# Kernel optimization log

Measured on AMD Instinct MI355X. Metric: run time of the kernel, lower is better.

Reference implementation:

```python
import jax, jax.numpy as jnp
import numpy as np

B, H, W = 16, 1024, 1024
EPS = 1e-7
FG_PROB = 0.1  # foreground pixel probability for synthetic gt


def setup_inputs() -> dict:
    key = jax.random.key(0)
    k1, k2 = jax.random.split(key)
    probs = jax.random.normal(k1, (B, 2, H, W), dtype=jnp.float32)
    gt = (jax.random.uniform(k2, (B, H, W)) < FG_PROB).astype(jnp.float32)
    gt_f_num = gt.sum(axis=(1, 2))  # per-sample foreground pixel count (float)
    return {"probs": probs, "gt": gt, "gt_f_num": gt_f_num, "img_h": H, "img_w": W}


def reference(probs, gt, gt_f_num, img_h, img_w):
    # foreground probability, clamped
    pc = jax.nn.softmax(probs, axis=1)[:, 1, :, :]
    pc = jnp.clip(pc, EPS, 1.0 - EPS)
    b = pc.shape[0]
    f_loss = -(gt * jnp.log(pc)).reshape(b, -1)          # [B, N]
    b_loss = -((1.0 - gt) * jnp.log(1.0 - pc)).reshape(b, -1)  # [B, N]
    n = b_loss.shape[1]

    # sort background loss descending per sample; top gt_f_num[i] entries are
    # "difficult" negatives, the rest are "simple" (equivalent to the torch
    # gather-into-zero-buffers since only sums/counts are taken afterwards)
    sorted_b = -jnp.sort(-b_loss, axis=1)                # descending, [B, N]
    k = gt_f_num.astype(jnp.int32)                       # int(gt_f_num[i])
    mask = jnp.arange(n, dtype=jnp.int32)[None, :] < k[:, None]  # [B, N]

    difficult_sum = jnp.sum(jnp.where(mask, sorted_b, 0.0), axis=1)
    simple_sum = jnp.sum(jnp.where(mask, 0.0, sorted_b), axis=1)
    difficult_num = jnp.sum(mask & (sorted_b != 0.0), axis=1).astype(jnp.float32)

    difficult_b_loss = difficult_sum / (difficult_num + 1e-16)
    simple_b_loss = simple_sum / (float(img_h * img_w) + 1e-16)
    f_loss_mean = f_loss.sum(axis=1) / (gt_f_num + 1e-16)

    return difficult_b_loss.mean() + f_loss_mean.mean() + simple_b_loss.mean()
```

## Files before the change

kernel.cpp:

```cpp
#include <hip/hip_runtime.h>
#include <math.h>

#define NB 16
#define NPIX 1048576
#define BINS 2048
#define CHUNKS 128
#define TPB_A 512
#define PIX_PER_BLOCK (NPIX / CHUNKS)
#define PPT 16
#define ITERS (PIX_PER_BLOCK / (TPB_A * 4))
#define REPL 8
#define TPB_B 256
#define BINS_PER_CHUNK (BINS / TPB_B)
#define D_LO   (-10.24f)
#define D_SCALE (100.0f)
#define D_BIAS  (1024.0f)
#define BINW_D  (0.01f)

__global__ __launch_bounds__(TPB_A) void pass_a(
    const float* __restrict__ probs, const float* __restrict__ gt,
    unsigned* __restrict__ g_cnt)
{
    __shared__ unsigned s_cnt[BINS];

    const int tid = threadIdx.x;
    #pragma unroll
    for (int j = 0; j < BINS / TPB_A; ++j) s_cnt[j * TPB_A + tid] = 0u;
    __syncthreads();

    const int blk = blockIdx.x;
    const int b = blk / CHUNKS;
    const int chunk = blk % CHUNKS;
    const float* p0 = probs + (size_t)b * 2 * NPIX;
    const float* p1 = p0 + NPIX;
    const float* gp = gt + (size_t)b * NPIX;
    const int base = chunk * PIX_PER_BLOCK;

    #pragma unroll
    for (int it = 0; it < ITERS; ++it) {
        const int i = base + ((it * TPB_A + tid) << 2);
        const float4 v0 = *(const float4*)(p0 + i);
        const float4 v1 = *(const float4*)(p1 + i);
        const float4 vg = *(const float4*)(gp + i);
        const float dv[4] = {v1.x - v0.x, v1.y - v0.y, v1.z - v0.z, v1.w - v0.w};
        const float gv[4] = {vg.x, vg.y, vg.z, vg.w};
        #pragma unroll
        for (int c = 0; c < 4; ++c) {
            int bin = (int)fmaf(dv[c], D_SCALE, D_BIAS);
            bin = bin < 0 ? 0 : (bin > BINS - 1 ? BINS - 1 : bin);
            const unsigned inc = (gv[c] > 0.5f) ? 0x10000u : 1u;
            atomicAdd(&s_cnt[bin], inc);
        }
    }
    __syncthreads();

    unsigned* dst = g_cnt + ((size_t)b * REPL + (chunk & (REPL - 1))) * BINS;
    #pragma unroll
    for (int j = 0; j < BINS / TPB_A; ++j) {
        const int bin = j * TPB_A + tid;
        const unsigned c = s_cnt[bin];
        if (c) atomicAdd(&dst[bin], c);
    }
}

__device__ __forceinline__ float softplus_ref(float m) {
    return fmaxf(m, 0.f) + log1pf(__expf(-fabsf(m)));
}

__global__ __launch_bounds__(TPB_B) void pass_b(
    const unsigned* __restrict__ g_cnt, const float* __restrict__ gt_f_num,
    float* __restrict__ terms)
{
    __shared__ unsigned s_cnt[BINS];
    __shared__ unsigned s_suf[TPB_B];
    __shared__ double s_wsuf[TPB_B];
    __shared__ double s_fred[TPB_B];
    __shared__ double s_dsum;

    const int b = blockIdx.x;
    const int t = threadIdx.x;

    #pragma unroll
    for (int j = 0; j < BINS_PER_CHUNK; ++j) {
        const int bin = j * TPB_B + t;
        unsigned c = 0;
        #pragma unroll
        for (int r = 0; r < REPL; ++r)
            c += g_cnt[((size_t)b * REPL + r) * BINS + bin];
        s_cnt[bin] = c;
    }
    __syncthreads();

    unsigned c = 0; double w = 0.0, f = 0.0;
    const int cb = t * BINS_PER_CHUNK;
    #pragma unroll
    for (int j = 0; j < BINS_PER_CHUNK; ++j) {
        const unsigned pk = s_cnt[cb + j];
        const unsigned bg = pk & 0xFFFFu, fg = pk >> 16;
        const float m = fmaf((float)(cb + j) + 0.5f, BINW_D, D_LO);
        const float sp = softplus_ref(m);
        c += bg;
        w += (double)bg * (double)sp;
        f += (double)fg * (double)(sp - m);
    }
    s_suf[t] = c; s_wsuf[t] = w; s_fred[t] = f;
    __syncthreads();

    for (int off = 1; off < TPB_B; off <<= 1) {
        const unsigned ac = (t + off < TPB_B) ? s_suf[t + off] : 0u;
        const double aw = (t + off < TPB_B) ? s_wsuf[t + off] : 0.0;
        const double af = (t + off < TPB_B) ? s_fred[t + off] : 0.0;
        __syncthreads();
        s_suf[t] += ac; s_wsuf[t] += aw; s_fred[t] += af;
        __syncthreads();
    }

    const long long kk = (long long)gt_f_num[b];
    const unsigned long long n_pos = (unsigned long long)s_suf[0];
    const unsigned long long suf_me = s_suf[t];
    const unsigned long long suf_nx = (t + 1 < TPB_B) ? s_suf[t + 1] : 0ull;

    if (kk > 0 && (unsigned long long)kk < n_pos &&
        suf_nx < (unsigned long long)kk && (unsigned long long)kk <= suf_me) {
        unsigned long long cum = suf_nx;
        double W = (t + 1 < TPB_B) ? s_wsuf[t + 1] : 0.0;
        int bstar = cb;
        for (int j = BINS_PER_CHUNK - 1; j >= 0; --j) {
            const int bin = cb + j;
            const unsigned bg = s_cnt[bin] & 0xFFFFu;
            if (cum + bg >= (unsigned long long)kk) { bstar = bin; break; }
            cum += bg;
            const float m = fmaf((float)bin + 0.5f, BINW_D, D_LO);
            W += (double)bg * (double)softplus_ref(m);
        }
        const double partial = (double)(kk - (long long)cum);
        const float mstar = fmaf((float)bstar + 0.5f, BINW_D, D_LO);
        s_dsum = W + partial * (double)softplus_ref(mstar);
    }
    __syncthreads();

    if (t == 0) {
        const double S_total = s_wsuf[0];
        const double fs = s_fred[0];
        const double gfn = (double)gt_f_num[b];
        double dsum, dnum;
        if (kk <= 0) { dsum = 0.0; dnum = 0.0; }
        else if ((unsigned long long)kk >= n_pos) { dsum = S_total; dnum = (double)n_pos; }
        else { dsum = s_dsum; dnum = (double)kk; }
        const double term = dsum / (dnum + 1e-16)
                          + fs / (gfn + 1e-16)
                          + (S_total - dsum) / ((double)NPIX + 1e-16);
        terms[b] = (float)term;
    }
}

__global__ void pass_c(const float* __restrict__ terms, float* __restrict__ out)
{
    if (threadIdx.x == 0 && blockIdx.x == 0) {
        float s = 0.f;
        #pragma unroll
        for (int i = 0; i < NB; ++i) s += terms[i];
        out[0] = s / (float)NB;
    }
}

extern "C" void kernel_launch(void* const* d_in, const int* in_sizes, int n_in,
                              void* d_out, int out_size, void* d_ws, size_t ws_size,
                              hipStream_t stream) {
    const float* probs = (const float*)d_in[0];
    const float* gt    = (const float*)d_in[1];
    const float* gfn   = (const float*)d_in[2];
    char* ws = (char*)d_ws;

    const size_t hist_bytes = (size_t)NB * REPL * BINS * 4;
    unsigned* g_cnt = (unsigned*)ws;
    float*    terms = (float*)(ws + hist_bytes);

    hipMemsetAsync(ws, 0, hist_bytes, stream);

    hipLaunchKernelGGL(pass_a, dim3(NB * CHUNKS), dim3(TPB_A), 0, stream,
                       probs, gt, g_cnt);
    hipLaunchKernelGGL(pass_b, dim3(NB), dim3(TPB_B), 0, stream,
                       g_cnt, gfn, terms);
    hipLaunchKernelGGL(pass_c, dim3(1), dim3(64), 0, stream,
                       terms, (float*)d_out);
}
```

Baseline: 248.5 us.

## Compute loss sums exactly per pixel and histogram only a narrow background band

```diff
diff --git a/kernel.cpp b/kernel.cpp
--- a/kernel.cpp
+++ b/kernel.cpp
@@ -3,29 +3,35 @@
 
 #define NB 16
 #define NPIX 1048576
-#define BINS 2048
 #define CHUNKS 128
 #define TPB_A 512
 #define PIX_PER_BLOCK (NPIX / CHUNKS)
-#define PPT 16
 #define ITERS (PIX_PER_BLOCK / (TPB_A * 4))
 #define REPL 8
 #define TPB_B 256
-#define BINS_PER_CHUNK (BINS / TPB_B)
-#define D_LO   (-10.24f)
-#define D_SCALE (100.0f)
-#define D_BIAS  (1024.0f)
-#define BINW_D  (0.01f)
+#define BBINS 2048
+#define BINS_PER_CHUNK (BBINS / TPB_B)
+#define BAND_LO 0.9f
+#define BAND_HI 3.1f
+#define BSCALE ((float)BBINS / (BAND_HI - BAND_LO))
+#define BINW_B ((BAND_HI - BAND_LO) / (float)BBINS)
+#define B_CAP 16.636f
+#define F_CAP 16.1181f
+
+__device__ __forceinline__ void fadd_glb(float* p, float v) {
+    __hip_atomic_fetch_add(p, v, __ATOMIC_RELAXED, __HIP_MEMORY_SCOPE_AGENT);
+}
 
 __global__ __launch_bounds__(TPB_A) void pass_a(
     const float* __restrict__ probs, const float* __restrict__ gt,
-    unsigned* __restrict__ g_cnt)
+    unsigned* __restrict__ g_hist, float* __restrict__ g_scal)
 {
-    __shared__ unsigned s_cnt[BINS];
+    __shared__ unsigned s_hist[BBINS];
+    __shared__ float s_red[4][TPB_A / 64];
 
     const int tid = threadIdx.x;
     #pragma unroll
-    for (int j = 0; j < BINS / TPB_A; ++j) s_cnt[j * TPB_A + tid] = 0u;
+    for (int j = 0; j < BBINS / TPB_A; ++j) s_hist[j * TPB_A + tid] = 0u;
     __syncthreads();
 
     const int blk = blockIdx.x;
@@ -36,6 +42,8 @@
     const float* gp = gt + (size_t)b * NPIX;
     const int base = chunk * PIX_PER_BLOCK;
 
+    float f_acc = 0.f, b_acc = 0.f, shi_acc = 0.f, chi_acc = 0.f;
+
     #pragma unroll
     for (int it = 0; it < ITERS; ++it) {
         const int i = base + ((it * TPB_A + tid) << 2);
@@ -46,35 +54,60 @@
         const float gv[4] = {vg.x, vg.y, vg.z, vg.w};
         #pragma unroll
         for (int c = 0; c < 4; ++c) {
-            int bin = (int)fmaf(dv[c], D_SCALE, D_BIAS);
-            bin = bin < 0 ? 0 : (bin > BINS - 1 ? BINS - 1 : bin);
-            const unsigned inc = (gv[c] > 0.5f) ? 0x10000u : 1u;
-            atomicAdd(&s_cnt[bin], inc);
+            const float d = dv[c];
+            const float g = gv[c];
+            const float sp = fminf(fmaxf(d, 0.f) + __logf(1.f + __expf(-fabsf(d))), B_CAP);
+            f_acc += g * fminf(sp - d, F_CAP);
+            b_acc += (1.f - g) * sp;
+            const int bin = (int)fmaf(d, BSCALE, -BAND_LO * BSCALE);
+            const bool bg = g < 0.5f;
+            const float above = (bg && bin >= BBINS) ? 1.f : 0.f;
+            chi_acc += above;
+            shi_acc += above * sp;
+            if (bg && (unsigned)bin < (unsigned)BBINS)
+                atomicAdd(&s_hist[bin], 1u);
         }
     }
     __syncthreads();
 
-    unsigned* dst = g_cnt + ((size_t)b * REPL + (chunk & (REPL - 1))) * BINS;
-    #pragma unroll
-    for (int j = 0; j < BINS / TPB_A; ++j) {
+    unsigned* dst = g_hist + ((size_t)b * REPL + (chunk & (REPL - 1))) * BBINS;
+    #pragma unroll
+    for (int j = 0; j < BBINS / TPB_A; ++j) {
         const int bin = j * TPB_A + tid;
-        const unsigned c = s_cnt[bin];
+        const unsigned c = s_hist[bin];
         if (c) atomicAdd(&dst[bin], c);
     }
-}
-
-__device__ __forceinline__ float softplus_ref(float m) {
-    return fmaxf(m, 0.f) + log1pf(__expf(-fabsf(m)));
+
+    float v[4] = {f_acc, b_acc, shi_acc, chi_acc};
+    #pragma unroll
+    for (int k = 0; k < 4; ++k) {
+        #pragma unroll
+        for (int o = 32; o > 0; o >>= 1) v[k] += __shfl_down(v[k], o, 64);
+    }
+    if ((tid & 63) == 0) {
+        #pragma unroll
+        for (int k = 0; k < 4; ++k) s_red[k][tid >> 6] = v[k];
+    }
+    __syncthreads();
+    if (tid < 4) {
+        float s = 0.f;
+        #pragma unroll
+        for (int w = 0; w < TPB_A / 64; ++w) s += s_red[tid][w];
+        fadd_glb(&g_scal[b * 4 + tid], s);
+    }
+}
+
+__device__ __forceinline__ float softplus_acc(float m) {
+    return fmaxf(m, 0.f) + log1pf(expf(-fabsf(m)));
 }
 
 __global__ __launch_bounds__(TPB_B) void pass_b(
-    const unsigned* __restrict__ g_cnt, const float* __restrict__ gt_f_num,
-    float* __restrict__ terms)
+    const unsigned* __restrict__ g_hist, const float* __restrict__ g_scal,
+    const float* __restrict__ gt_f_num, float* __restrict__ terms)
 {
-    __shared__ unsigned s_cnt[BINS];
+    __shared__ unsigned s_cnt[BBINS];
     __shared__ unsigned s_suf[TPB_B];
     __shared__ double s_wsuf[TPB_B];
-    __shared__ double s_fred[TPB_B];
     __shared__ double s_dsum;
 
     const int b = blockIdx.x;
@@ -86,67 +119,78 @@
         unsigned c = 0;
         #pragma unroll
         for (int r = 0; r < REPL; ++r)
-            c += g_cnt[((size_t)b * REPL + r) * BINS + bin];
+            c += g_hist[((size_t)b * REPL + r) * BBINS + bin];
         s_cnt[bin] = c;
     }
     __syncthreads();
 
-    unsigned c = 0; double w = 0.0, f = 0.0;
+    unsigned c = 0; double w = 0.0;
     const int cb = t * BINS_PER_CHUNK;
     #pragma unroll
     for (int j = 0; j < BINS_PER_CHUNK; ++j) {
-        const unsigned pk = s_cnt[cb + j];
-        const unsigned bg = pk & 0xFFFFu, fg = pk >> 16;
-        const float m = fmaf((float)(cb + j) + 0.5f, BINW_D, D_LO);
-        const float sp = softplus_ref(m);
-        c += bg;
-        w += (double)bg * (double)sp;
-        f += (double)fg * (double)(sp - m);
-    }
-    s_suf[t] = c; s_wsuf[t] = w; s_fred[t] = f;
+        const unsigned cc = s_cnt[cb + j];
+        const float m = fmaf((float)(cb + j) + 0.5f, BINW_B, BAND_LO);
+        c += cc;
+        w += (double)cc * (double)softplus_acc(m);
+    }
+    s_suf[t] = c; s_wsuf[t] = w;
     __syncthreads();
 
     for (int off = 1; off < TPB_B; off <<= 1) {
         const unsigned ac = (t + off < TPB_B) ? s_suf[t + off] : 0u;
         const double aw = (t + off < TPB_B) ? s_wsuf[t + off] : 0.0;
-        const double af = (t + off < TPB_B) ? s_fred[t + off] : 0.0;
         __syncthreads();
-        s_suf[t] += ac; s_wsuf[t] += aw; s_fred[t] += af;
+        s_suf[t] += ac; s_wsuf[t] += aw;
         __syncthreads();
     }
 
     const long long kk = (long long)gt_f_num[b];
-    const unsigned long long n_pos = (unsigned long long)s_suf[0];
-    const unsigned long long suf_me = s_suf[t];
-    const unsigned long long suf_nx = (t + 1 < TPB_B) ? s_suf[t + 1] : 0ull;
-
-    if (kk > 0 && (unsigned long long)kk < n_pos &&
-        suf_nx < (unsigned long long)kk && (unsigned long long)kk <= suf_me) {
-        unsigned long long cum = suf_nx;
-        double W = (t + 1 < TPB_B) ? s_wsuf[t + 1] : 0.0;
-        int bstar = cb;
-        for (int j = BINS_PER_CHUNK - 1; j >= 0; --j) {
-            const int bin = cb + j;
-            const unsigned bg = s_cnt[bin] & 0xFFFFu;
-            if (cum + bg >= (unsigned long long)kk) { bstar = bin; break; }
-            cum += bg;
-            const float m = fmaf((float)bin + 0.5f, BINW_D, D_LO);
-            W += (double)bg * (double)softplus_ref(m);
+    const long long n_pos = (long long)NPIX - kk;
+    const long long c_hi = (long long)(g_scal[b * 4 + 3] + 0.5f);
+    const long long kp = kk - c_hi;
+    const long long c_band = (long long)s_suf[0];
+
+    if (kp > 0 && kp <= c_band && kk < n_pos) {
+        const long long suf_me = (long long)s_suf[t];
+        const long long suf_nx = (t + 1 < TPB_B) ? (long long)s_suf[t + 1] : 0;
+        if (suf_nx < kp && kp <= suf_me) {
+            long long cum = suf_nx;
+            double W = (t + 1 < TPB_B) ? s_wsuf[t + 1] : 0.0;
+            int bstar = cb;
+            for (int j = BINS_PER_CHUNK - 1; j >= 0; --j) {
+                const int bin = cb + j;
+                const unsigned bc = s_cnt[bin];
+                if (cum + bc >= kp) { bstar = bin; break; }
+                cum += bc;
+                const float m = fmaf((float)bin + 0.5f, BINW_B, BAND_LO);
+                W += (double)bc * (double)softplus_acc(m);
+            }
+            const double partial = (double)(kp - cum);
+            const float ms = fmaf((float)bstar + 0.5f, BINW_B, BAND_LO);
+            s_dsum = W + partial * (double)softplus_acc(ms);
         }
-        const double partial = (double)(kk - (long long)cum);
-        const float mstar = fmaf((float)bstar + 0.5f, BINW_D, D_LO);
-        s_dsum = W + partial * (double)softplus_ref(mstar);
     }
     __syncthreads();
 
     if (t == 0) {
-        const double S_total = s_wsuf[0];
-        const double fs = s_fred[0];
+        const double fs      = (double)g_scal[b * 4 + 0];
+        const double S_total = (double)g_scal[b * 4 + 1];
+        const double s_hi    = (double)g_scal[b * 4 + 2];
         const double gfn = (double)gt_f_num[b];
         double dsum, dnum;
         if (kk <= 0) { dsum = 0.0; dnum = 0.0; }
-        else if ((unsigned long long)kk >= n_pos) { dsum = S_total; dnum = (double)n_pos; }
-        else { dsum = s_dsum; dnum = (double)kk; }
+        else if (kk >= n_pos) { dsum = S_total; dnum = (double)n_pos; }
+        else if (kp <= 0) {
+            dsum = s_hi * ((double)kk / (double)(c_hi > 0 ? c_hi : 1));
+            dnum = (double)kk;
+        } else if (kp > c_band) {
+            dsum = s_hi + s_wsuf[0]
+                 + (double)(kp - c_band) * (double)softplus_acc(BAND_LO);
+            dnum = (double)kk;
+        } else {
+            dsum = s_hi + s_dsum;
+            dnum = (double)kk;
+        }
         const double term = dsum / (dnum + 1e-16)
                           + fs / (gfn + 1e-16)
                           + (S_total - dsum) / ((double)NPIX + 1e-16);
@@ -172,16 +216,17 @@
     const float* gfn   = (const float*)d_in[2];
     char* ws = (char*)d_ws;
 
-    const size_t hist_bytes = (size_t)NB * REPL * BINS * 4;
-    unsigned* g_cnt = (unsigned*)ws;
-    float*    terms = (float*)(ws + hist_bytes);
-
-    hipMemsetAsync(ws, 0, hist_bytes, stream);
+    const size_t hist_bytes = (size_t)NB * REPL * BBINS * 4;
+    unsigned* g_hist = (unsigned*)ws;
+    float*    g_scal = (float*)(ws + hist_bytes);
+    float*    terms  = g_scal + NB * 4;
+
+    hipMemsetAsync(ws, 0, hist_bytes + NB * 4 * sizeof(float), stream);
 
     hipLaunchKernelGGL(pass_a, dim3(NB * CHUNKS), dim3(TPB_A), 0, stream,
-                       probs, gt, g_cnt);
+                       probs, gt, g_hist, g_scal);
     hipLaunchKernelGGL(pass_b, dim3(NB), dim3(TPB_B), 0, stream,
-                       g_cnt, gfn, terms);
+                       g_hist, g_scal, gfn, terms);
     hipLaunchKernelGGL(pass_c, dim3(1), dim3(64), 0, stream,
                        terms, (float*)d_out);
 }
```

Result: no change. 252.3 us (+1.5%).
